# Kernel tuning notes

Measured on AMD Instinct MI355X. Metric: run time of the kernel, lower is better.

Reference implementation:

```python
import jax, jax.numpy as jnp
import numpy as np

B, S, D, H = 1, 4096, 1024, 16
HD = D // H  # head_dim = 64
NEG = -1e9

def setup_inputs() -> dict:
    key = jax.random.key(0)
    ks = jax.random.split(key, 5)
    scale = 1.0 / np.sqrt(D)
    x = jax.random.normal(ks[0], (B, S, D), dtype=jnp.float32)
    Wq = jax.random.normal(ks[1], (D, D), dtype=jnp.float32) * scale
    Wk = jax.random.normal(ks[2], (D, D), dtype=jnp.float32) * scale
    Wv = jax.random.normal(ks[3], (D, D), dtype=jnp.float32) * scale
    Wo = jax.random.normal(ks[4], (D, D), dtype=jnp.float32) * scale
    mask = jnp.tril(jnp.ones((S, S), dtype=bool))[None, None]  # [1,1,S,S] causal
    return {"x": x, "mask": mask, "Wq": Wq, "Wk": Wk, "Wv": Wv, "Wo": Wo}

def reference(x, mask, Wq, Wk, Wv, Wo):
    # Linear projections (bias=False). nn.Linear computes x @ W.T; weights here
    # are stored as [out, in] so we use x @ W.T for faithfulness.
    q = x @ Wq.T  # [B,S,D]
    k = x @ Wk.T
    v = x @ Wv.T
    def split_heads(t):
        return t.reshape(B, S, H, HD).transpose(0, 2, 1, 3)  # [B,H,S,HD]
    q, k, v = split_heads(q), split_heads(k), split_heads(v)
    scores = jnp.einsum("bhqd,bhkd->bhqk", q, k) / jnp.sqrt(jnp.float32(HD))
    scores = jnp.where(mask, scores, NEG)
    attn = jax.nn.softmax(scores, axis=-1)  # dropout p=0.0 -> identity
    out = jnp.einsum("bhqk,bhkd->bhqd", attn, v)  # [B,H,S,HD]
    out = out.transpose(0, 2, 1, 3).reshape(B, S, D)
    return out @ Wo.T
```

## Files before the change

### kernel.cpp

```cpp
#include <hip/hip_runtime.h>
#include <hip/hip_bf16.h>


typedef __bf16 bf16x8 __attribute__((ext_vector_type(8)));
typedef __bf16 bf16x4 __attribute__((ext_vector_type(4)));
typedef float f32x4 __attribute__((ext_vector_type(4)));
typedef short s16x4 __attribute__((ext_vector_type(4)));

#define GAS __attribute__((address_space(1)))
#define LAS __attribute__((address_space(3)))

__device__ __forceinline__ void async_copy16(const void* g, void* l) {
  __builtin_amdgcn_global_load_lds((const GAS unsigned int*)g,
                                   (LAS unsigned int*)l, 16, 0, 0);
}

__device__ __forceinline__ f32x4 mfma_k16(bf16x4 a, bf16x4 b, f32x4 c) {
  union { bf16x4 h; s16x4 s; } ua, ub;
  ua.h = a; ub.h = b;
  return __builtin_amdgcn_mfma_f32_16x16x16bf16_1k(ua.s, ub.s, c, 0, 0, 0);
}

__global__ __launch_bounds__(256) void cvt_all(const float* __restrict__ x,
                                               const float* __restrict__ Wq,
                                               const float* __restrict__ Wk,
                                               const float* __restrict__ Wv,
                                               const float* __restrict__ Wo,
                                               __bf16* __restrict__ xb,
                                               __bf16* __restrict__ Wc,
                                               __bf16* __restrict__ Wob) {
  int b = blockIdx.x;
  const float* src;
  __bf16* dst;
  if (b < 4096)      { src = x  + (b       ) * 1024; dst = xb  + (long)b * 1024; }
  else if (b < 5120) { src = Wq + (b - 4096) * 1024; dst = Wc  + (long)(b - 4096) * 1024; }
  else if (b < 6144) { src = Wk + (b - 5120) * 1024; dst = Wc  + (1l << 20) + (long)(b - 5120) * 1024; }
  else if (b < 7168) { src = Wv + (b - 6144) * 1024; dst = Wc  + (2l << 20) + (long)(b - 6144) * 1024; }
  else               { src = Wo + (b - 7168) * 1024; dst = Wob + (long)(b - 7168) * 1024; }
  int i = threadIdx.x * 4;
  float4 f = *(const float4*)(src + i);
  bf16x4 o;
  o[0] = (__bf16)f.x; o[1] = (__bf16)f.y; o[2] = (__bf16)f.z; o[3] = (__bf16)f.w;
  *(bf16x4*)(dst + i) = o;
}

__global__ __launch_bounds__(256) void gemm_qkv(const __bf16* __restrict__ A,
                                                const __bf16* __restrict__ B,
                                                __bf16* __restrict__ Qb,
                                                __bf16* __restrict__ Kf,
                                                __bf16* __restrict__ Vf) {
  const int K = 1024;
  __shared__ __bf16 As[128 * 32];
  __shared__ __bf16 Bs[128 * 32];
  const int tid = threadIdx.x;
  const int lane = tid & 63, wv = tid >> 6;
  const int l15 = lane & 15, quad = lane >> 4;
  const int wm = wv >> 1, wn = wv & 1;
  const int mbase = blockIdx.y * 128, nbase = blockIdx.x * 128;
  const bool kswap = (nbase >= 1024) && (nbase < 2048);

  f32x4 acc[4][4] = {};

  for (int k0 = 0; k0 < K; k0 += 32) {
    __syncthreads();
#pragma unroll
    for (int q = 0; q < 2; ++q) {
      int i = q * 256 + tid;
      int row = i >> 2, kg = i & 3;
      const __bf16* ga = A + (long)(mbase + row) * K + k0 + kg * 8;
      const __bf16* gb = B + (long)(nbase + row) * K + k0 + kg * 8;
      char* la = (char*)As + (q * 256 + wv * 64) * 16;
      char* lb = (char*)Bs + (q * 256 + wv * 64) * 16;
      async_copy16(ga, la);
      async_copy16(gb, lb);
    }
    __syncthreads();
    bf16x8 af[4], bfr[4];
#pragma unroll
    for (int i = 0; i < 4; ++i)
      af[i] = *(const bf16x8*)&As[(wm * 64 + i * 16 + l15) * 32 + quad * 8];
#pragma unroll
    for (int j = 0; j < 4; ++j)
      bfr[j] = *(const bf16x8*)&Bs[(wn * 64 + j * 16 + l15) * 32 + quad * 8];
    if (kswap) {
#pragma unroll
      for (int i = 0; i < 4; ++i)
#pragma unroll
        for (int j = 0; j < 4; ++j)
          acc[i][j] = __builtin_amdgcn_mfma_f32_16x16x32_bf16(bfr[j], af[i], acc[i][j], 0, 0, 0);
    } else {
#pragma unroll
      for (int i = 0; i < 4; ++i)
#pragma unroll
        for (int j = 0; j < 4; ++j)
          acc[i][j] = __builtin_amdgcn_mfma_f32_16x16x32_bf16(af[i], bfr[j], acc[i][j], 0, 0, 0);
    }
  }

  if (nbase < 1024) {
    const float QS = 0.18033688011112043f;
#pragma unroll
    for (int i = 0; i < 4; ++i)
#pragma unroll
      for (int j = 0; j < 4; ++j) {
        int col = nbase + wn * 64 + j * 16 + l15;
#pragma unroll
        for (int r = 0; r < 4; ++r) {
          int row = mbase + wm * 64 + i * 16 + quad * 4 + r;
          Qb[(long)row * 1024 + col] = (__bf16)(acc[i][j][r] * QS);
        }
      }
  } else if (nbase < 2048) {
#pragma unroll
    for (int i = 0; i < 4; ++i)
#pragma unroll
      for (int j = 0; j < 4; ++j) {
        int d0 = nbase - 1024 + wn * 64 + j * 16 + quad * 4;
        int h = d0 >> 6, dd = d0 & 63;
        int kk = dd >> 5, qf = (dd >> 3) & 3, e0 = dd & 7;
        int kt = mbase + wm * 64 + i * 16 + l15;
        int tile = kt >> 6;
        long off = ((long)(h * 64 + tile) * 8 + i * 2 + kk) * 512 + (qf * 16 + l15) * 8 + e0;
        union { __bf16 b[4]; uint2 u; } pk;
#pragma unroll
        for (int r = 0; r < 4; ++r) pk.b[r] = (__bf16)acc[i][j][r];
        *(uint2*)(Kf + off) = pk.u;
      }
  } else {
#pragma unroll
    for (int i = 0; i < 4; ++i)
#pragma unroll
      for (int j = 0; j < 4; ++j) {
        int col = nbase - 2048 + wn * 64 + j * 16 + l15;
        int h = col >> 6, dd = col & 63;
        int jd = dd >> 4, lv = dd & 15;
        int kt0 = mbase + wm * 64 + i * 16 + quad * 4;
        int tile = kt0 >> 6, w6 = kt0 & 63;
        int jp = w6 >> 5, bit4 = (w6 >> 4) & 1, qv = (w6 >> 2) & 3;
        long off = ((long)(h * 64 + tile) * 8 + jd * 2 + jp) * 512 + (qv * 16 + lv) * 8 + bit4 * 4;
        union { __bf16 b[4]; uint2 u; } pk;
#pragma unroll
        for (int r = 0; r < 4; ++r) pk.b[r] = (__bf16)acc[i][j][r];
        *(uint2*)(Vf + off) = pk.u;
      }
  }
}

__global__ __launch_bounds__(256) void gemm_wo(const __bf16* __restrict__ A,
                                               const __bf16* __restrict__ B,
                                               float* __restrict__ C) {
  const int K = 1024, N = 1024;
  __shared__ __bf16 As[128 * 32];
  __shared__ __bf16 Bs[64 * 32];
  const int tid = threadIdx.x;
  const int lane = tid & 63, wv = tid >> 6;
  const int l15 = lane & 15, quad = lane >> 4;
  const int wm = wv >> 1, wn = wv & 1;
  const int mbase = blockIdx.y * 128, nbase = blockIdx.x * 64;

  f32x4 acc[4][2] = {};

  for (int k0 = 0; k0 < K; k0 += 32) {
    __syncthreads();
#pragma unroll
    for (int q = 0; q < 2; ++q) {
      int i = q * 256 + tid;
      int row = i >> 2, kg = i & 3;
      const __bf16* ga = A + (long)(mbase + row) * K + k0 + kg * 8;
      char* la = (char*)As + (q * 256 + wv * 64) * 16;
      async_copy16(ga, la);
    }
    {
      int row = tid >> 2, kg = tid & 3;
      const __bf16* gb = B + (long)(nbase + row) * K + k0 + kg * 8;
      char* lb = (char*)Bs + (wv * 64) * 16;
      async_copy16(gb, lb);
    }
    __syncthreads();
    bf16x8 af[4], bfr[2];
#pragma unroll
    for (int i = 0; i < 4; ++i)
      af[i] = *(const bf16x8*)&As[(wm * 64 + i * 16 + l15) * 32 + quad * 8];
#pragma unroll
    for (int j = 0; j < 2; ++j)
      bfr[j] = *(const bf16x8*)&Bs[(wn * 32 + j * 16 + l15) * 32 + quad * 8];
#pragma unroll
    for (int i = 0; i < 4; ++i)
#pragma unroll
      for (int j = 0; j < 2; ++j)
        acc[i][j] = __builtin_amdgcn_mfma_f32_16x16x32_bf16(af[i], bfr[j], acc[i][j], 0, 0, 0);
  }
#pragma unroll
  for (int i = 0; i < 4; ++i)
#pragma unroll
    for (int j = 0; j < 2; ++j)
#pragma unroll
      for (int r = 0; r < 4; ++r) {
        int row = mbase + wm * 64 + i * 16 + quad * 4 + r;
        int col = nbase + wn * 32 + j * 16 + l15;
        C[(long)row * N + col] = acc[i][j][r];
      }
}

__global__ __launch_bounds__(512, 2) void flash_attn(const __bf16* __restrict__ Qb,
                                                     const __bf16* __restrict__ Kf,
                                                     const __bf16* __restrict__ Vf,
                                                     __bf16* __restrict__ AO) {
  __shared__ float Ms[4][64][35];
  const int tid = threadIdx.x;
  const int lane = tid & 63, l15 = lane & 15, quad = lane >> 4;
  const int w = tid >> 6;
  const int pr = w >> 1, half = w & 1;
  const int b = blockIdx.x;
  const int h = (b & 7) + 8 * ((b >> 3) & 1);
  const int rest = b >> 4;
  const int P = rest * 4 + pr;
  const int hoff = h * 64;

  const __bf16* Kh = Kf + (long)h * 64 * 4096;
  const __bf16* Vh = Vf + (long)h * 64 * 4096;

  for (int pass = 0; pass < 2; ++pass) {
    const int T = pass ? (127 - P) : P;
    bf16x8 qf[2][2];
#pragma unroll
    for (int g = 0; g < 2; ++g) {
      const int qrow = T * 32 + g * 16 + l15;
      qf[g][0] = *(const bf16x8*)(Qb + (long)qrow * 1024 + hoff + quad * 8);
      qf[g][1] = *(const bf16x8*)(Qb + (long)qrow * 1024 + hoff + 32 + quad * 8);
    }

    const int nkt = (T >> 1) + 1;
    const int kt0 = half ? (nkt >> 1) : 0;
    const int kt1 = half ? nkt : (nkt >> 1);
    f32x4 o_acc[2][4] = {};
    float l_acc[2] = {0.0f, 0.0f};

    bf16x8 kc[8];
    if (kt0 < kt1) {
      const __bf16* Kt = Kh + (long)kt0 * 4096;
#pragma unroll
      for (int f = 0; f < 8; ++f)
        kc[f] = *(const bf16x8*)(Kt + f * 512 + lane * 8);
    }

    for (int kt = kt0; kt < kt1; ++kt) {
      const __bf16* Vt = Vh + (long)kt * 4096;

      bf16x8 va[8];
#pragma unroll
      for (int f = 0; f < 8; ++f)
        va[f] = *(const bf16x8*)(Vt + f * 512 + lane * 8);

      f32x4 st[2][4] = {};
#pragma unroll
      for (int g = 0; g < 2; ++g)
#pragma unroll
        for (int j = 0; j < 4; ++j) {
          st[g][j] = __builtin_amdgcn_mfma_f32_16x16x32_bf16(kc[j * 2 + 0], qf[g][0], st[g][j], 0, 0, 0);
          st[g][j] = __builtin_amdgcn_mfma_f32_16x16x32_bf16(kc[j * 2 + 1], qf[g][1], st[g][j], 0, 0, 0);
        }

      if (kt + 1 < kt1) {
        const __bf16* Kt = Kh + (long)(kt + 1) * 4096;
#pragma unroll
        for (int f = 0; f < 8; ++f)
          kc[f] = *(const bf16x8*)(Kt + f * 512 + lane * 8);
      }

      if (kt == nkt - 1) {
#pragma unroll
        for (int g = 0; g < 2; ++g) {
          const int dq = (T & 1) * 32 + g * 16 + l15;
#pragma unroll
          for (int j = 0; j < 4; ++j)
#pragma unroll
            for (int r = 0; r < 4; ++r)
              if (j * 16 + quad * 4 + r > dq) st[g][j][r] = -3.0e38f;
        }
      }

      bf16x4 pb[2][4];
#pragma unroll
      for (int g = 0; g < 2; ++g) {
        float ps = 0.0f;
#pragma unroll
        for (int j = 0; j < 4; ++j) {
          f32x4 pj;
#pragma unroll
          for (int r = 0; r < 4; ++r) pj[r] = __builtin_amdgcn_exp2f(st[g][j][r]);
          ps += (pj[0] + pj[1]) + (pj[2] + pj[3]);
          bf16x4 bb;
#pragma unroll
          for (int r = 0; r < 4; ++r) bb[r] = (__bf16)pj[r];
          pb[g][j] = bb;
        }
        l_acc[g] += ps;
      }

#pragma unroll
      for (int g = 0; g < 2; ++g)
#pragma unroll
        for (int j = 0; j < 4; ++j) {
          bf16x4 pbj = pb[g][j];
#pragma unroll
          for (int jd = 0; jd < 4; ++jd) {
            bf16x8 v8 = va[jd * 2 + (j >> 1)];
            bf16x4 a4 = (j & 1) ? __builtin_shufflevector(v8, v8, 4, 5, 6, 7)
                                : __builtin_shufflevector(v8, v8, 0, 1, 2, 3);
            o_acc[g][jd] = mfma_k16(a4, pbj, o_acc[g][jd]);
          }
        }
    }

    if (half) {
#pragma unroll
      for (int g = 0; g < 2; ++g) {
#pragma unroll
        for (int jd = 0; jd < 4; ++jd)
#pragma unroll
          for (int r = 0; r < 4; ++r)
            Ms[pr][lane][g * 16 + jd * 4 + r] = o_acc[g][jd][r];
        Ms[pr][lane][32 + g] = l_acc[g];
      }
    }
    __syncthreads();
    if (!half) {
#pragma unroll
      for (int g = 0; g < 2; ++g) {
#pragma unroll
        for (int jd = 0; jd < 4; ++jd)
#pragma unroll
          for (int r = 0; r < 4; ++r)
            o_acc[g][jd][r] += Ms[pr][lane][g * 16 + jd * 4 + r];
        float la = l_acc[g] + Ms[pr][lane][32 + g];
        la += __shfl_xor(la, 16);
        la += __shfl_xor(la, 32);
        const float inv = 1.0f / la;
        const int qrow = T * 32 + g * 16 + l15;
#pragma unroll
        for (int jd = 0; jd < 4; ++jd) {
          bf16x4 ob;
#pragma unroll
          for (int r = 0; r < 4; ++r) ob[r] = (__bf16)(o_acc[g][jd][r] * inv);
          *(bf16x4*)(AO + (long)qrow * 1024 + hoff + jd * 16 + quad * 4) = ob;
        }
      }
    }
    __syncthreads();
  }
}

extern "C" void kernel_launch(void* const* d_in, const int* in_sizes, int n_in,
                              void* d_out, int out_size, void* d_ws, size_t ws_size,
                              hipStream_t stream) {
  const float* x  = (const float*)d_in[0];
  const float* Wq = (const float*)d_in[2];
  const float* Wk = (const float*)d_in[3];
  const float* Wv = (const float*)d_in[4];
  const float* Wo = (const float*)d_in[5];
  float* out = (float*)d_out;

  char* ws = (char*)d_ws;
  __bf16* xb  = (__bf16*)ws;
  __bf16* Wc  = (__bf16*)(ws + (8u << 20));
  __bf16* Wob = (__bf16*)(ws + (14u << 20));
  __bf16* Qb  = (__bf16*)(ws + (16u << 20));
  __bf16* Kfr = (__bf16*)(ws + (24u << 20));
  __bf16* Vfr = (__bf16*)(ws + (32u << 20));
  __bf16* AO  = (__bf16*)(ws + (40u << 20));

  cvt_all<<<8192, 256, 0, stream>>>(x, Wq, Wk, Wv, Wo, xb, Wc, Wob);

  dim3 g1(3072 / 128, 4096 / 128);
  gemm_qkv<<<g1, 256, 0, stream>>>(xb, Wc, Qb, Kfr, Vfr);

  flash_attn<<<256, 512, 0, stream>>>(Qb, Kfr, Vfr, AO);

  dim3 g2(1024 / 64, 4096 / 128);
  gemm_wo<<<g2, 256, 0, stream>>>(AO, Wob, out);
}
```

Measured before the change: 232.4 us.

## Split attention KV range four ways and vectorize GEMM output stores

The flash attention kernel now splits each query tile's key range across four waves instead of two. Each block handles two query tiles, the grid doubles to 512 blocks, and the occupancy hint rises to 4 blocks per CU. Partial outputs and row sums from three waves are reduced through shared memory. Separately, the Q projection and Wo GEMM swap their MFMA operands so each lane holds contiguous columns, letting the epilogues write packed 8-byte or 16-byte stores instead of scalar ones. The extra reduction adds shared-memory traffic, and the higher occupancy target may constrain registers.

```diff
diff --git a/kernel.cpp b/kernel.cpp
--- a/kernel.cpp
+++ b/kernel.cpp
@@ -57,7 +57,7 @@
   const int l15 = lane & 15, quad = lane >> 4;
   const int wm = wv >> 1, wn = wv & 1;
   const int mbase = blockIdx.y * 128, nbase = blockIdx.x * 128;
-  const bool kswap = (nbase >= 1024) && (nbase < 2048);
+  const bool swp = (nbase < 2048);
 
   f32x4 acc[4][4] = {};
 
@@ -82,7 +82,7 @@
 #pragma unroll
     for (int j = 0; j < 4; ++j)
       bfr[j] = *(const bf16x8*)&Bs[(wn * 64 + j * 16 + l15) * 32 + quad * 8];
-    if (kswap) {
+    if (swp) {
 #pragma unroll
       for (int i = 0; i < 4; ++i)
 #pragma unroll
@@ -100,16 +100,17 @@
   if (nbase < 1024) {
     const float QS = 0.18033688011112043f;
 #pragma unroll
-    for (int i = 0; i < 4; ++i)
+    for (int i = 0; i < 4; ++i) {
+      int row = mbase + wm * 64 + i * 16 + l15;
 #pragma unroll
       for (int j = 0; j < 4; ++j) {
-        int col = nbase + wn * 64 + j * 16 + l15;
-#pragma unroll
-        for (int r = 0; r < 4; ++r) {
-          int row = mbase + wm * 64 + i * 16 + quad * 4 + r;
-          Qb[(long)row * 1024 + col] = (__bf16)(acc[i][j][r] * QS);
-        }
-      }
+        int cb = nbase + wn * 64 + j * 16 + quad * 4;
+        union { __bf16 b[4]; uint2 u; } pk;
+#pragma unroll
+        for (int r = 0; r < 4; ++r) pk.b[r] = (__bf16)(acc[i][j][r] * QS);
+        *(uint2*)(Qb + (long)row * 1024 + cb) = pk.u;
+      }
+    }
   } else if (nbase < 2048) {
 #pragma unroll
     for (int i = 0; i < 4; ++i)
@@ -188,33 +189,32 @@
     for (int i = 0; i < 4; ++i)
 #pragma unroll
       for (int j = 0; j < 2; ++j)
-        acc[i][j] = __builtin_amdgcn_mfma_f32_16x16x32_bf16(af[i], bfr[j], acc[i][j], 0, 0, 0);
-  }
-#pragma unroll
-  for (int i = 0; i < 4; ++i)
-#pragma unroll
-    for (int j = 0; j < 2; ++j)
-#pragma unroll
-      for (int r = 0; r < 4; ++r) {
-        int row = mbase + wm * 64 + i * 16 + quad * 4 + r;
-        int col = nbase + wn * 32 + j * 16 + l15;
-        C[(long)row * N + col] = acc[i][j][r];
-      }
-}
-
-__global__ __launch_bounds__(512, 2) void flash_attn(const __bf16* __restrict__ Qb,
+        acc[i][j] = __builtin_amdgcn_mfma_f32_16x16x32_bf16(bfr[j], af[i], acc[i][j], 0, 0, 0);
+  }
+#pragma unroll
+  for (int i = 0; i < 4; ++i) {
+    int row = mbase + wm * 64 + i * 16 + l15;
+#pragma unroll
+    for (int j = 0; j < 2; ++j) {
+      int cb = nbase + wn * 32 + j * 16 + quad * 4;
+      *(f32x4*)(C + (long)row * N + cb) = acc[i][j];
+    }
+  }
+}
+
+__global__ __launch_bounds__(512, 4) void flash_attn(const __bf16* __restrict__ Qb,
                                                      const __bf16* __restrict__ Kf,
                                                      const __bf16* __restrict__ Vf,
                                                      __bf16* __restrict__ AO) {
-  __shared__ float Ms[4][64][35];
+  __shared__ float Ms[2][3][64][34];
   const int tid = threadIdx.x;
   const int lane = tid & 63, l15 = lane & 15, quad = lane >> 4;
   const int w = tid >> 6;
-  const int pr = w >> 1, half = w & 1;
+  const int pr = w >> 2, qtr = w & 3;
   const int b = blockIdx.x;
   const int h = (b & 7) + 8 * ((b >> 3) & 1);
   const int rest = b >> 4;
-  const int P = rest * 4 + pr;
+  const int P = rest * 2 + pr;
   const int hoff = h * 64;
 
   const __bf16* Kh = Kf + (long)h * 64 * 4096;
@@ -231,8 +231,8 @@
     }
 
     const int nkt = (T >> 1) + 1;
-    const int kt0 = half ? (nkt >> 1) : 0;
-    const int kt1 = half ? nkt : (nkt >> 1);
+    const int kt0 = (nkt * qtr) >> 2;
+    const int kt1 = (nkt * (qtr + 1)) >> 2;
     f32x4 o_acc[2][4] = {};
     float l_acc[2] = {0.0f, 0.0f};
 
@@ -313,27 +313,29 @@
         }
     }
 
-    if (half) {
+    if (qtr) {
 #pragma unroll
       for (int g = 0; g < 2; ++g) {
 #pragma unroll
         for (int jd = 0; jd < 4; ++jd)
 #pragma unroll
           for (int r = 0; r < 4; ++r)
-            Ms[pr][lane][g * 16 + jd * 4 + r] = o_acc[g][jd][r];
-        Ms[pr][lane][32 + g] = l_acc[g];
-      }
-    }
-    __syncthreads();
-    if (!half) {
+            Ms[pr][qtr - 1][lane][g * 16 + jd * 4 + r] = o_acc[g][jd][r];
+        Ms[pr][qtr - 1][lane][32 + g] = l_acc[g];
+      }
+    }
+    __syncthreads();
+    if (!qtr) {
 #pragma unroll
       for (int g = 0; g < 2; ++g) {
 #pragma unroll
-        for (int jd = 0; jd < 4; ++jd)
-#pragma unroll
-          for (int r = 0; r < 4; ++r)
-            o_acc[g][jd][r] += Ms[pr][lane][g * 16 + jd * 4 + r];
-        float la = l_acc[g] + Ms[pr][lane][32 + g];
+        for (int s = 0; s < 3; ++s)
+#pragma unroll
+          for (int jd = 0; jd < 4; ++jd)
+#pragma unroll
+            for (int r = 0; r < 4; ++r)
+              o_acc[g][jd][r] += Ms[pr][s][lane][g * 16 + jd * 4 + r];
+        float la = l_acc[g] + Ms[pr][0][lane][32 + g] + Ms[pr][1][lane][32 + g] + Ms[pr][2][lane][32 + g];
         la += __shfl_xor(la, 16);
         la += __shfl_xor(la, 32);
         const float inv = 1.0f / la;
@@ -375,7 +377,7 @@
   dim3 g1(3072 / 128, 4096 / 128);
   gemm_qkv<<<g1, 256, 0, stream>>>(xb, Wc, Qb, Kfr, Vfr);
 
-  flash_attn<<<256, 512, 0, stream>>>(Qb, Kfr, Vfr, AO);
+  flash_attn<<<512, 512, 0, stream>>>(Qb, Kfr, Vfr, AO);
 
   dim3 g2(1024 / 64, 4096 / 128);
   gemm_wo<<<g2, 256, 0, stream>>>(AO, Wob, out);
```

After: 472.7 us. +103.4%, slower.
